# Performance work log

Measured on AMD Instinct MI355X. Metric: run time of the kernel, lower is better.

## Reference

```python
import jax, jax.numpy as jnp
import numpy as np

B = 16        # number of lists
N = 1024      # items per list (all equal)
D = 256       # feature dim (= dim_emb, need_embedding=False)


def setup_inputs() -> dict:
    key = jax.random.key(0)
    k1, k2, k3 = jax.random.split(key, 3)
    feats = jax.random.normal(k1, (B * N, D), dtype=jnp.float32)
    length = jnp.full((B,), N, dtype=jnp.int32)
    # Bilinear params: torch nn.Bilinear(d, d, 1) -> weight [1, d, d], bias [1]
    # xavier_uniform on the 3-d weight: bound = sqrt(6 / (fan_in + fan_out)) with
    # fan_in = d (last dim), fan_out = 1*d (per torch _calculate_fan_in_and_fan_out)
    bound = float(np.sqrt(6.0 / (D + D)))
    W_upper = jax.random.uniform(k2, (1, D, D), jnp.float32, -bound, bound)
    W_lower = jax.random.uniform(k3, (1, D, D), jnp.float32, -bound, bound)
    b_upper = jnp.zeros((1,), jnp.float32)
    b_lower = jnp.zeros((1,), jnp.float32)
    return {"feats": feats, "W_upper": W_upper, "b_upper": b_upper,
            "W_lower": W_lower, "b_lower": b_lower, "length": length}


def reference(feats, W_upper, b_upper, W_lower, b_lower, length):
    # nb_layers=0, need_embedding=False -> embedding and transformer are Identity.
    b = length.shape[0]
    n = feats.shape[0] // b  # equal-length lists -> static reshape
    d = feats.shape[-1]
    X = feats.reshape(b, n, d)  # [B, n, d]
    # For list i: repeated_feats_1 row (p*n + q) = x_p, repeated_feats_2 row = x_q,
    # so adjacency[p, q] = x_p^T W x_q + bias  (Bilinear with out=1).
    upper = jnp.einsum('bnd,de,bme->bnm', X, W_upper[0], X) + b_upper[0]
    lower = jnp.einsum('bnd,de,bme->bnm', X, W_lower[0], X) + b_lower[0]
    adj = jnp.triu(upper) + jnp.tril(lower, -1)  # [B, n, n]
    return adj
```

## Files before the change

kernel.cpp:

```cpp
#include <hip/hip_runtime.h>

#define BL 16
#define NL 1024
#define DD 256

typedef short bf16x8 __attribute__((ext_vector_type(8)));
typedef float f32x4 __attribute__((ext_vector_type(4)));

static __device__ __forceinline__ short f32_to_bf16(float f) {
  union { float f; unsigned u; } v; v.f = f;
  unsigned r = (v.u + 0x7FFFu + ((v.u >> 16) & 1u)) >> 16;
  return (short)r;
}

static __device__ __forceinline__ void g2l16(const short* g, short* l) {
  __builtin_amdgcn_global_load_lds(
      (const __attribute__((address_space(1))) void*)g,
      (__attribute__((address_space(3))) void*)l, 16, 0, 0);
}

static __device__ __forceinline__ void stage_tile(const short* __restrict__ gbase,
                                                  short* __restrict__ lds,
                                                  int t, int k0) {
  const int row = t >> 2, kc = t & 3;
#pragma unroll
  for (int i = 0; i < 2; ++i) {
    const short* g = gbase + (size_t)(row + 64 * i) * DD + k0 + kc * 8;
    g2l16(g, lds + i * 2048 + t * 8);
  }
}

static __device__ __forceinline__ void mma_step(const short* __restrict__ As,
                                                const short* __restrict__ Bs,
                                                int wm, int wn, int r, int quad,
                                                f32x4 acc[4][4]) {
  bf16x8 af[4], bf[4];
#pragma unroll
  for (int i = 0; i < 4; ++i) {
    af[i] = *(const bf16x8*)(As + (wm + i * 16 + r) * 32 + quad * 8);
    bf[i] = *(const bf16x8*)(Bs + (wn + i * 16 + r) * 32 + quad * 8);
  }
#pragma unroll
  for (int mt = 0; mt < 4; ++mt)
#pragma unroll
    for (int nt = 0; nt < 4; ++nt)
      acc[mt][nt] = __builtin_amdgcn_mfma_f32_16x16x32_bf16(af[mt], bf[nt], acc[mt][nt], 0, 0, 0);
}

__global__ __launch_bounds__(256) void k_prep(const float* __restrict__ X,
                                              const float* __restrict__ Wu,
                                              const float* __restrict__ Wl,
                                              short* __restrict__ Xb,
                                              short* __restrict__ WTu,
                                              short* __restrict__ WTl) {
  const int bid = blockIdx.x;
  if (bid < 4096) {
    int i = bid * 256 + threadIdx.x;
    const float4 v = ((const float4*)X)[i];
    short4 o;
    o.x = f32_to_bf16(v.x); o.y = f32_to_bf16(v.y);
    o.z = f32_to_bf16(v.z); o.w = f32_to_bf16(v.w);
    ((short4*)Xb)[i] = o;
  } else {
    const int id = bid - 4096;
    const int z = id >> 8, d = id & 255;
    const float* W = z ? Wl : Wu;
    short* WT = z ? WTl : WTu;
    const int e = threadIdx.x;
    WT[e * DD + d] = f32_to_bf16(W[d * DD + e]);
  }
}

__global__ __launch_bounds__(256) void k_stage1(const short* __restrict__ Xb,
                                                const short* __restrict__ WTu,
                                                const short* __restrict__ WTl,
                                                short* __restrict__ YU,
                                                short* __restrict__ YL) {
  __shared__ short As[2][128 * 32], Bs[2][128 * 32];
  const short* Bt = blockIdx.z ? WTl : WTu;
  short* Y = blockIdx.z ? YL : YU;
  const int m0 = blockIdx.y * 128, n0 = blockIdx.x * 128;
  const int t = threadIdx.x, lane = t & 63, wave = t >> 6;
  const int r = lane & 15, quad = lane >> 4;
  const int wm = (wave >> 1) * 64, wn = (wave & 1) * 64;
  f32x4 acc[4][4] = {};
  const short* Ag = Xb + (size_t)m0 * DD;
  const short* Bg = Bt + (size_t)n0 * DD;
  for (int k0 = 0; k0 < DD; k0 += 64) {
    stage_tile(Ag, As[0], t, k0);
    stage_tile(Ag, As[1], t, k0 + 32);
    stage_tile(Bg, Bs[0], t, k0);
    stage_tile(Bg, Bs[1], t, k0 + 32);
    __syncthreads();
    mma_step(As[0], Bs[0], wm, wn, r, quad, acc);
    mma_step(As[1], Bs[1], wm, wn, r, quad, acc);
    __syncthreads();
  }
#pragma unroll
  for (int mt = 0; mt < 4; ++mt)
#pragma unroll
    for (int nt = 0; nt < 4; ++nt)
#pragma unroll
      for (int i = 0; i < 4; ++i)
        Y[(size_t)(m0 + wm + mt * 16 + quad * 4 + i) * DD + n0 + wn + nt * 16 + r] =
            f32_to_bf16(acc[mt][nt][i]);
}

__global__ __launch_bounds__(256) void k_stage2_off(const short* __restrict__ Xb,
                                                    const short* __restrict__ YU,
                                                    const short* __restrict__ YL,
                                                    const float* __restrict__ bu_p,
                                                    const float* __restrict__ bl_p,
                                                    float* __restrict__ out) {
  __shared__ short As[2][128 * 32], Bs[2][128 * 32];
  const int idx = blockIdx.x, b = blockIdx.y;
  const int pt = idx / 7, j = idx % 7;
  const int qt = j + (j >= pt ? 1 : 0);
  const size_t off = (size_t)b * NL * DD;
  const short* Ag = ((qt > pt) ? YU : YL) + off + (size_t)pt * 128 * DD;
  const short* Bg = Xb + off + (size_t)qt * 128 * DD;
  const float bias = (qt > pt) ? bu_p[0] : bl_p[0];
  const int t = threadIdx.x, lane = t & 63, wave = t >> 6;
  const int r = lane & 15, quad = lane >> 4;
  const int wm = (wave >> 1) * 64, wn = (wave & 1) * 64;
  const f32x4 binit = {bias, bias, bias, bias};
  f32x4 acc[4][4];
#pragma unroll
  for (int mt = 0; mt < 4; ++mt)
#pragma unroll
    for (int nt = 0; nt < 4; ++nt) acc[mt][nt] = binit;
  for (int k0 = 0; k0 < DD; k0 += 64) {
    stage_tile(Ag, As[0], t, k0);
    stage_tile(Ag, As[1], t, k0 + 32);
    stage_tile(Bg, Bs[0], t, k0);
    stage_tile(Bg, Bs[1], t, k0 + 32);
    __syncthreads();
    mma_step(As[0], Bs[0], wm, wn, r, quad, acc);
    mma_step(As[1], Bs[1], wm, wn, r, quad, acc);
    __syncthreads();
  }
  float* Ob = out + (size_t)b * NL * NL;
  const int p0 = pt * 128 + wm, q0 = qt * 128 + wn;
#pragma unroll
  for (int mt = 0; mt < 4; ++mt)
#pragma unroll
    for (int nt = 0; nt < 4; ++nt)
#pragma unroll
      for (int i = 0; i < 4; ++i)
        Ob[(size_t)(p0 + mt * 16 + quad * 4 + i) * NL + q0 + nt * 16 + r] =
            acc[mt][nt][i];
}

__global__ __launch_bounds__(256) void k_stage2_diag(const short* __restrict__ Xb,
                                                     const short* __restrict__ YU,
                                                     const short* __restrict__ YL,
                                                     const float* __restrict__ bu_p,
                                                     const float* __restrict__ bl_p,
                                                     float* __restrict__ out) {
  __shared__ short Au[2][128 * 32], Al[2][128 * 32], Bs[2][128 * 32];
  const int pt = blockIdx.x, b = blockIdx.y;
  const size_t off = (size_t)b * NL * DD;
  const short* Agu = YU + off + (size_t)pt * 128 * DD;
  const short* Agl = YL + off + (size_t)pt * 128 * DD;
  const short* Bg = Xb + off + (size_t)pt * 128 * DD;
  const float bu = bu_p[0], bl = bl_p[0];
  const int t = threadIdx.x, lane = t & 63, wave = t >> 6;
  const int r = lane & 15, quad = lane >> 4;
  const int wm = (wave >> 1) * 64, wn = (wave & 1) * 64;
  f32x4 accU[4][4] = {}, accL[4][4] = {};
  for (int k0 = 0; k0 < DD; k0 += 64) {
    stage_tile(Agu, Au[0], t, k0);
    stage_tile(Agu, Au[1], t, k0 + 32);
    stage_tile(Agl, Al[0], t, k0);
    stage_tile(Agl, Al[1], t, k0 + 32);
    stage_tile(Bg, Bs[0], t, k0);
    stage_tile(Bg, Bs[1], t, k0 + 32);
    __syncthreads();
    mma_step(Au[0], Bs[0], wm, wn, r, quad, accU);
    mma_step(Al[0], Bs[0], wm, wn, r, quad, accL);
    mma_step(Au[1], Bs[1], wm, wn, r, quad, accU);
    mma_step(Al[1], Bs[1], wm, wn, r, quad, accL);
    __syncthreads();
  }
  float* Ob = out + (size_t)b * NL * NL;
  const int p0 = pt * 128 + wm, q0 = pt * 128 + wn;
#pragma unroll
  for (int mt = 0; mt < 4; ++mt)
#pragma unroll
    for (int nt = 0; nt < 4; ++nt)
#pragma unroll
      for (int i = 0; i < 4; ++i) {
        const int p = p0 + mt * 16 + quad * 4 + i;
        const int q = q0 + nt * 16 + r;
        Ob[(size_t)p * NL + q] =
            (q >= p) ? (accU[mt][nt][i] + bu) : (accL[mt][nt][i] + bl);
      }
}

extern "C" void kernel_launch(void* const* d_in, const int* in_sizes, int n_in,
                              void* d_out, int out_size, void* d_ws, size_t ws_size,
                              hipStream_t stream) {
  const float* feats = (const float*)d_in[0];
  const float* Wu    = (const float*)d_in[1];
  const float* bu    = (const float*)d_in[2];
  const float* Wl    = (const float*)d_in[3];
  const float* bl    = (const float*)d_in[4];
  float* out = (float*)d_out;

  char* ws = (char*)d_ws;
  short* Xb  = (short*)(ws);
  short* YU  = (short*)(ws + (size_t)8 * 1024 * 1024);
  short* YL  = (short*)(ws + (size_t)16 * 1024 * 1024);
  short* WTu = (short*)(ws + (size_t)24 * 1024 * 1024);
  short* WTl = (short*)(ws + (size_t)24 * 1024 * 1024 + DD * DD * 2);

  k_prep<<<4096 + 512, 256, 0, stream>>>(feats, Wu, Wl, Xb, WTu, WTl);

  k_stage1<<<dim3(DD / 128, BL * NL / 128, 2), 256, 0, stream>>>(Xb, WTu, WTl, YU, YL);

  k_stage2_off<<<dim3(56, BL), 256, 0, stream>>>(Xb, YU, YL, bu, bl, out);
  k_stage2_diag<<<dim3(8, BL), 256, 0, stream>>>(Xb, YU, YL, bu, bl, out);
}
```

Measured before the change: 134.1 us.

## Fuse both GEMM stages into one kernel keeping Y rows in LDS

Replaces the separate stage-1 and two stage-2 kernels with a single fused kernel. Each block computes its 64-row slice of X·Wu and X·Wl into swizzled LDS, then each wave streams X tiles straight from global memory to produce the output tiles. This removes the Y round trip through global memory and two kernel launches. In exchange it runs only 256 blocks, loads the B operand directly from global without LDS staging, and uses a large LDS footprint, which may limit occupancy and latency hiding.

```diff
diff --git a/kernel.cpp b/kernel.cpp
--- a/kernel.cpp
+++ b/kernel.cpp
@@ -17,34 +17,6 @@
   __builtin_amdgcn_global_load_lds(
       (const __attribute__((address_space(1))) void*)g,
       (__attribute__((address_space(3))) void*)l, 16, 0, 0);
-}
-
-static __device__ __forceinline__ void stage_tile(const short* __restrict__ gbase,
-                                                  short* __restrict__ lds,
-                                                  int t, int k0) {
-  const int row = t >> 2, kc = t & 3;
-#pragma unroll
-  for (int i = 0; i < 2; ++i) {
-    const short* g = gbase + (size_t)(row + 64 * i) * DD + k0 + kc * 8;
-    g2l16(g, lds + i * 2048 + t * 8);
-  }
-}
-
-static __device__ __forceinline__ void mma_step(const short* __restrict__ As,
-                                                const short* __restrict__ Bs,
-                                                int wm, int wn, int r, int quad,
-                                                f32x4 acc[4][4]) {
-  bf16x8 af[4], bf[4];
-#pragma unroll
-  for (int i = 0; i < 4; ++i) {
-    af[i] = *(const bf16x8*)(As + (wm + i * 16 + r) * 32 + quad * 8);
-    bf[i] = *(const bf16x8*)(Bs + (wn + i * 16 + r) * 32 + quad * 8);
-  }
-#pragma unroll
-  for (int mt = 0; mt < 4; ++mt)
-#pragma unroll
-    for (int nt = 0; nt < 4; ++nt)
-      acc[mt][nt] = __builtin_amdgcn_mfma_f32_16x16x32_bf16(af[mt], bf[nt], acc[mt][nt], 0, 0, 0);
 }
 
 __global__ __launch_bounds__(256) void k_prep(const float* __restrict__ X,
@@ -71,130 +43,129 @@
   }
 }
 
-__global__ __launch_bounds__(256) void k_stage1(const short* __restrict__ Xb,
-                                                const short* __restrict__ WTu,
-                                                const short* __restrict__ WTl,
-                                                short* __restrict__ YU,
-                                                short* __restrict__ YL) {
-  __shared__ short As[2][128 * 32], Bs[2][128 * 32];
-  const short* Bt = blockIdx.z ? WTl : WTu;
-  short* Y = blockIdx.z ? YL : YU;
-  const int m0 = blockIdx.y * 128, n0 = blockIdx.x * 128;
-  const int t = threadIdx.x, lane = t & 63, wave = t >> 6;
-  const int r = lane & 15, quad = lane >> 4;
-  const int wm = (wave >> 1) * 64, wn = (wave & 1) * 64;
+static __device__ __forceinline__ void tile_pass(const short* __restrict__ Ylds,
+                                                 const short* __restrict__ Bg,
+                                                 float* __restrict__ Ob,
+                                                 int p0, int q0, float bias,
+                                                 int mode, int r, int quad) {
   f32x4 acc[4][4] = {};
-  const short* Ag = Xb + (size_t)m0 * DD;
-  const short* Bg = Bt + (size_t)n0 * DD;
-  for (int k0 = 0; k0 < DD; k0 += 64) {
-    stage_tile(Ag, As[0], t, k0);
-    stage_tile(Ag, As[1], t, k0 + 32);
-    stage_tile(Bg, Bs[0], t, k0);
-    stage_tile(Bg, Bs[1], t, k0 + 32);
-    __syncthreads();
-    mma_step(As[0], Bs[0], wm, wn, r, quad, acc);
-    mma_step(As[1], Bs[1], wm, wn, r, quad, acc);
-    __syncthreads();
+#pragma unroll
+  for (int ks = 0; ks < 8; ++ks) {
+    bf16x8 af[4], bf[4];
+#pragma unroll
+    for (int mt = 0; mt < 4; ++mt) {
+      const int row = mt * 16 + r;
+      const int byte = (row * 512 + ks * 64 + quad * 16) ^ ((row & 7) << 4);
+      af[mt] = *(const bf16x8*)((const char*)Ylds + byte);
+    }
+#pragma unroll
+    for (int nt = 0; nt < 4; ++nt)
+      bf[nt] = *(const bf16x8*)(Bg + (size_t)(nt * 16 + r) * DD + ks * 32 + quad * 8);
+#pragma unroll
+    for (int mt = 0; mt < 4; ++mt)
+#pragma unroll
+      for (int nt = 0; nt < 4; ++nt)
+        acc[mt][nt] = __builtin_amdgcn_mfma_f32_16x16x32_bf16(af[mt], bf[nt],
+                                                              acc[mt][nt], 0, 0, 0);
   }
 #pragma unroll
   for (int mt = 0; mt < 4; ++mt)
 #pragma unroll
-    for (int nt = 0; nt < 4; ++nt)
-#pragma unroll
-      for (int i = 0; i < 4; ++i)
-        Y[(size_t)(m0 + wm + mt * 16 + quad * 4 + i) * DD + n0 + wn + nt * 16 + r] =
-            f32_to_bf16(acc[mt][nt][i]);
-}
-
-__global__ __launch_bounds__(256) void k_stage2_off(const short* __restrict__ Xb,
-                                                    const short* __restrict__ YU,
-                                                    const short* __restrict__ YL,
-                                                    const float* __restrict__ bu_p,
-                                                    const float* __restrict__ bl_p,
-                                                    float* __restrict__ out) {
-  __shared__ short As[2][128 * 32], Bs[2][128 * 32];
-  const int idx = blockIdx.x, b = blockIdx.y;
-  const int pt = idx / 7, j = idx % 7;
-  const int qt = j + (j >= pt ? 1 : 0);
-  const size_t off = (size_t)b * NL * DD;
-  const short* Ag = ((qt > pt) ? YU : YL) + off + (size_t)pt * 128 * DD;
-  const short* Bg = Xb + off + (size_t)qt * 128 * DD;
-  const float bias = (qt > pt) ? bu_p[0] : bl_p[0];
-  const int t = threadIdx.x, lane = t & 63, wave = t >> 6;
-  const int r = lane & 15, quad = lane >> 4;
-  const int wm = (wave >> 1) * 64, wn = (wave & 1) * 64;
-  const f32x4 binit = {bias, bias, bias, bias};
-  f32x4 acc[4][4];
-#pragma unroll
-  for (int mt = 0; mt < 4; ++mt)
-#pragma unroll
-    for (int nt = 0; nt < 4; ++nt) acc[mt][nt] = binit;
-  for (int k0 = 0; k0 < DD; k0 += 64) {
-    stage_tile(Ag, As[0], t, k0);
-    stage_tile(Ag, As[1], t, k0 + 32);
-    stage_tile(Bg, Bs[0], t, k0);
-    stage_tile(Bg, Bs[1], t, k0 + 32);
-    __syncthreads();
-    mma_step(As[0], Bs[0], wm, wn, r, quad, acc);
-    mma_step(As[1], Bs[1], wm, wn, r, quad, acc);
-    __syncthreads();
-  }
-  float* Ob = out + (size_t)b * NL * NL;
-  const int p0 = pt * 128 + wm, q0 = qt * 128 + wn;
-#pragma unroll
-  for (int mt = 0; mt < 4; ++mt)
-#pragma unroll
-    for (int nt = 0; nt < 4; ++nt)
-#pragma unroll
-      for (int i = 0; i < 4; ++i)
-        Ob[(size_t)(p0 + mt * 16 + quad * 4 + i) * NL + q0 + nt * 16 + r] =
-            acc[mt][nt][i];
-}
-
-__global__ __launch_bounds__(256) void k_stage2_diag(const short* __restrict__ Xb,
-                                                     const short* __restrict__ YU,
-                                                     const short* __restrict__ YL,
-                                                     const float* __restrict__ bu_p,
-                                                     const float* __restrict__ bl_p,
-                                                     float* __restrict__ out) {
-  __shared__ short Au[2][128 * 32], Al[2][128 * 32], Bs[2][128 * 32];
-  const int pt = blockIdx.x, b = blockIdx.y;
-  const size_t off = (size_t)b * NL * DD;
-  const short* Agu = YU + off + (size_t)pt * 128 * DD;
-  const short* Agl = YL + off + (size_t)pt * 128 * DD;
-  const short* Bg = Xb + off + (size_t)pt * 128 * DD;
-  const float bu = bu_p[0], bl = bl_p[0];
-  const int t = threadIdx.x, lane = t & 63, wave = t >> 6;
-  const int r = lane & 15, quad = lane >> 4;
-  const int wm = (wave >> 1) * 64, wn = (wave & 1) * 64;
-  f32x4 accU[4][4] = {}, accL[4][4] = {};
-  for (int k0 = 0; k0 < DD; k0 += 64) {
-    stage_tile(Agu, Au[0], t, k0);
-    stage_tile(Agu, Au[1], t, k0 + 32);
-    stage_tile(Agl, Al[0], t, k0);
-    stage_tile(Agl, Al[1], t, k0 + 32);
-    stage_tile(Bg, Bs[0], t, k0);
-    stage_tile(Bg, Bs[1], t, k0 + 32);
-    __syncthreads();
-    mma_step(Au[0], Bs[0], wm, wn, r, quad, accU);
-    mma_step(Al[0], Bs[0], wm, wn, r, quad, accL);
-    mma_step(Au[1], Bs[1], wm, wn, r, quad, accU);
-    mma_step(Al[1], Bs[1], wm, wn, r, quad, accL);
-    __syncthreads();
-  }
-  float* Ob = out + (size_t)b * NL * NL;
-  const int p0 = pt * 128 + wm, q0 = pt * 128 + wn;
-#pragma unroll
-  for (int mt = 0; mt < 4; ++mt)
-#pragma unroll
-    for (int nt = 0; nt < 4; ++nt)
+    for (int nt = 0; nt < 4; ++nt) {
+      const int q = q0 + nt * 16 + r;
 #pragma unroll
       for (int i = 0; i < 4; ++i) {
         const int p = p0 + mt * 16 + quad * 4 + i;
-        const int q = q0 + nt * 16 + r;
-        Ob[(size_t)p * NL + q] =
-            (q >= p) ? (accU[mt][nt][i] + bu) : (accL[mt][nt][i] + bl);
+        if (mode == 0 || (mode == 1 && q >= p) || (mode == 2 && q < p))
+          Ob[(size_t)p * NL + q] = acc[mt][nt][i] + bias;
       }
+    }
+}
+
+__global__ __launch_bounds__(512) void k_fused(const short* __restrict__ Xb,
+                                               const short* __restrict__ WTu,
+                                               const short* __restrict__ WTl,
+                                               const float* __restrict__ bu_p,
+                                               const float* __restrict__ bl_p,
+                                               float* __restrict__ out) {
+  __shared__ short Asw[64 * 256];
+  __shared__ short Yu[64 * 256];
+  __shared__ short Yl[64 * 256];
+
+  const int bid = blockIdx.x;
+  const int b = bid & 15, pt = bid >> 4;
+  const int t = threadIdx.x, lane = t & 63, w = t >> 6;
+  const int r = lane & 15, quad = lane >> 4;
+  const size_t listoff = (size_t)b * NL * DD;
+  const short* Ap = Xb + listoff + (size_t)pt * 64 * DD;
+
+#pragma unroll
+  for (int i = 0; i < 4; ++i) {
+    const int c = i * 512 + t;
+    const int src = (c & ~31) | ((c & 31) ^ ((c >> 5) & 7));
+    g2l16(Ap + src * 8, Asw + c * 8);
+  }
+  __syncthreads();
+
+  {
+    const int n0 = w * 32;
+    f32x4 aU[4][2] = {}, aL[4][2] = {};
+#pragma unroll
+    for (int ks = 0; ks < 8; ++ks) {
+      bf16x8 af[4], bfu[2], bfl[2];
+#pragma unroll
+      for (int mt = 0; mt < 4; ++mt) {
+        const int row = mt * 16 + r;
+        const int byte = (row * 512 + ks * 64 + quad * 16) ^ ((row & 7) << 4);
+        af[mt] = *(const bf16x8*)((const char*)Asw + byte);
+      }
+#pragma unroll
+      for (int nt = 0; nt < 2; ++nt) {
+        const int off = (n0 + nt * 16 + r) * DD + ks * 32 + quad * 8;
+        bfu[nt] = *(const bf16x8*)(WTu + off);
+        bfl[nt] = *(const bf16x8*)(WTl + off);
+      }
+#pragma unroll
+      for (int mt = 0; mt < 4; ++mt)
+#pragma unroll
+        for (int nt = 0; nt < 2; ++nt) {
+          aU[mt][nt] = __builtin_amdgcn_mfma_f32_16x16x32_bf16(af[mt], bfu[nt], aU[mt][nt], 0, 0, 0);
+          aL[mt][nt] = __builtin_amdgcn_mfma_f32_16x16x32_bf16(af[mt], bfl[nt], aL[mt][nt], 0, 0, 0);
+        }
+    }
+#pragma unroll
+    for (int mt = 0; mt < 4; ++mt)
+#pragma unroll
+      for (int nt = 0; nt < 2; ++nt)
+#pragma unroll
+        for (int i = 0; i < 4; ++i) {
+          const int row = mt * 16 + quad * 4 + i;
+          const int col = n0 + nt * 16 + r;
+          const int byte = (row * 512 + col * 2) ^ ((row & 7) << 4);
+          *(short*)((char*)Yu + byte) = f32_to_bf16(aU[mt][nt][i]);
+          *(short*)((char*)Yl + byte) = f32_to_bf16(aL[mt][nt][i]);
+        }
+  }
+  __syncthreads();
+
+  const float ubias = bu_p[0], lbias = bl_p[0];
+  float* Ob = out + (size_t)b * NL * NL;
+  const short* Bglist = Xb + listoff;
+  const int p0 = pt * 64;
+
+  for (int qq = 0; qq < 2; ++qq) {
+    const int qt = w + qq * 8;
+    const short* Bg = Bglist + (size_t)qt * 64 * DD;
+    const int q0 = qt * 64;
+    if (qt > pt) {
+      tile_pass(Yu, Bg, Ob, p0, q0, ubias, 0, r, quad);
+    } else if (qt < pt) {
+      tile_pass(Yl, Bg, Ob, p0, q0, lbias, 0, r, quad);
+    } else {
+      tile_pass(Yu, Bg, Ob, p0, q0, ubias, 1, r, quad);
+      tile_pass(Yl, Bg, Ob, p0, q0, lbias, 2, r, quad);
+    }
+  }
 }
 
 extern "C" void kernel_launch(void* const* d_in, const int* in_sizes, int n_in,
@@ -209,15 +180,10 @@
 
   char* ws = (char*)d_ws;
   short* Xb  = (short*)(ws);
-  short* YU  = (short*)(ws + (size_t)8 * 1024 * 1024);
-  short* YL  = (short*)(ws + (size_t)16 * 1024 * 1024);
-  short* WTu = (short*)(ws + (size_t)24 * 1024 * 1024);
-  short* WTl = (short*)(ws + (size_t)24 * 1024 * 1024 + DD * DD * 2);
+  short* WTu = (short*)(ws + (size_t)8 * 1024 * 1024);
+  short* WTl = (short*)(ws + (size_t)8 * 1024 * 1024 + DD * DD * 2);
 
   k_prep<<<4096 + 512, 256, 0, stream>>>(feats, Wu, Wl, Xb, WTu, WTl);
 
-  k_stage1<<<dim3(DD / 128, BL * NL / 128, 2), 256, 0, stream>>>(Xb, WTu, WTl, YU, YL);
-
-  k_stage2_off<<<dim3(56, BL), 256, 0, stream>>>(Xb, YU, YL, bu, bl, out);
-  k_stage2_diag<<<dim3(8, BL), 256, 0, stream>>>(Xb, YU, YL, bu, bl, out);
+  k_fused<<<256, 512, 0, stream>>>(Xb, WTu, WTl, bu, bl, out);
 }
```

Result: slower. 143.9 us (+7.2%).
